# Performance work log

Measured on AMD Instinct MI355X. Metric: run time of the kernel, lower is better.

The kernel has to match this reference:

```python
import jax, jax.numpy as jnp
import numpy as np

HIDDEN = 1024
HEADS = 16
HEAD_DIM = HIDDEN // HEADS


def setup_inputs() -> dict:
    key = jax.random.key(0)
    ks = jax.random.split(key, 9)
    s = 1.0 / np.sqrt(HIDDEN)
    x = jax.random.normal(ks[0], (1, 4096, HIDDEN), dtype=jnp.float32)
    return {
        "x": x,
        "wq": jax.random.normal(ks[1], (HIDDEN, HIDDEN), dtype=jnp.float32) * s,
        "bq": jnp.zeros((HIDDEN,), dtype=jnp.float32),
        "wk": jax.random.normal(ks[2], (HIDDEN, HIDDEN), dtype=jnp.float32) * s,
        "bk": jnp.zeros((HIDDEN,), dtype=jnp.float32),
        "wv": jax.random.normal(ks[3], (HIDDEN, HIDDEN), dtype=jnp.float32) * s,
        "bv": jnp.zeros((HIDDEN,), dtype=jnp.float32),
        "wo": jax.random.normal(ks[4], (HIDDEN, HIDDEN), dtype=jnp.float32) * s,
        "bo": jnp.zeros((HIDDEN,), dtype=jnp.float32),
    }


def reference(x, wq, bq, wk, bk, wv, bv, wo, bo):
    B, S, D = x.shape
    H, Hd = HEADS, HEAD_DIM
    # projections (torch Linear: y = x @ W.T + b)
    q = (x @ wq.T + bq).reshape(B, S, H, Hd).transpose(0, 2, 1, 3)  # [B,H,S,Hd]
    k = (x @ wk.T + bk).reshape(B, S, H, Hd).transpose(0, 2, 1, 3)
    v = (x @ wv.T + bv).reshape(B, S, H, Hd).transpose(0, 2, 1, 3)
    scores = jnp.einsum("bhqd,bhkd->bhqk", q, k) / jnp.sqrt(jnp.float32(Hd))
    attn = jax.nn.softmax(scores, axis=-1)  # full [B,H,S,S] matrix, faithful to source
    out = jnp.einsum("bhqk,bhkd->bhqd", attn, v)  # [B,H,S,Hd]
    out = out.transpose(0, 2, 1, 3).reshape(B, S, D)
    return out @ wo.T + bo
```

## Files before the change

kernel.cpp:

```cpp
#include <hip/hip_runtime.h>
#include <stdint.h>

#define S 4096
#define D 1024
#define H 16
#define HD 64

#define QK_SCALE 0.18033688011112042f

typedef short short8  __attribute__((ext_vector_type(8)));
typedef float floatx4 __attribute__((ext_vector_type(4)));
typedef float floatx16 __attribute__((ext_vector_type(16)));

__device__ __forceinline__ unsigned short f2bf(float f) {
  union { float f; unsigned int i; } x; x.f = f;
  unsigned int r = x.i + 0x7FFFu + ((x.i >> 16) & 1u);
  return (unsigned short)(r >> 16);
}

#if defined(__has_builtin)
#if __has_builtin(__builtin_amdgcn_cvt_pk_bf16_f32)
#define HAVE_PK_BF16 1
#endif
#if __has_builtin(__builtin_amdgcn_exp2f)
#define HAVE_RAW_EXP2 1
#endif
#endif

__device__ __forceinline__ unsigned int pkbf(float a, float b) {
#ifdef HAVE_PK_BF16
  typedef __bf16 bf2_t __attribute__((ext_vector_type(2)));
  bf2_t t = __builtin_amdgcn_cvt_pk_bf16_f32(a, b);
  return __builtin_bit_cast(unsigned int, t);
#else
  return (unsigned int)f2bf(a) | ((unsigned int)f2bf(b) << 16);
#endif
}

__device__ __forceinline__ float fexp2(float x) {
#ifdef HAVE_RAW_EXP2
  return __builtin_amdgcn_exp2f(x);
#else
  return exp2f(x);
#endif
}

__global__ __launch_bounds__(256) void cvt_kernel(
    const float* __restrict__ x,  unsigned short* __restrict__ xb,
    const float* __restrict__ wq, unsigned short* __restrict__ wqb,
    const float* __restrict__ wk, unsigned short* __restrict__ wkb,
    const float* __restrict__ wv, unsigned short* __restrict__ wvb,
    const float* __restrict__ wo, unsigned short* __restrict__ wob,
    const float* __restrict__ bq, float* __restrict__ bqs)
{
  const int z = blockIdx.y;
  const float* s; unsigned short* d;
  float scale = 1.f;
  if (z < 4)       { s = x + (size_t)z * 1048576; d = xb + (size_t)z * 1048576; }
  else if (z == 4) { s = wq; d = wqb; scale = QK_SCALE; }
  else if (z == 5) { s = wk; d = wkb; }
  else if (z == 6) { s = wv; d = wvb; }
  else             { s = wo; d = wob; }
  const size_t i = ((size_t)blockIdx.x * 256 + threadIdx.x) * 4;
  float4 v = *reinterpret_cast<const float4*>(s + i);
  uint2 o;
  o.x = pkbf(v.x * scale, v.y * scale);
  o.y = pkbf(v.z * scale, v.w * scale);
  *reinterpret_cast<uint2*>(d + i) = o;
  if (z == 4 && blockIdx.x == 0) {
    const int t = threadIdx.x;
    #pragma unroll
    for (int j = 0; j < 4; ++j) bqs[t * 4 + j] = bq[t * 4 + j] * QK_SCALE;
  }
}

__global__ __launch_bounds__(256) void gemm_bt(
    const unsigned short* __restrict__ X,
    const unsigned short* __restrict__ W0, const float* __restrict__ B0, unsigned short* __restrict__ C0,
    const unsigned short* __restrict__ W1, const float* __restrict__ B1, unsigned short* __restrict__ C1,
    const unsigned short* __restrict__ W2, const float* __restrict__ B2, unsigned short* __restrict__ C2,
    float* __restrict__ Cf, unsigned short* __restrict__ VtOut)
{
  const unsigned short* W; const float* Bb; unsigned short* C;
  const int z = blockIdx.z;
  if (z == 0)      { W = W0; Bb = B0; C = C0; }
  else if (z == 1) { W = W1; Bb = B1; C = C1; }
  else             { W = W2; Bb = B2; C = C2; }

  const int bm = blockIdx.y, bn = blockIdx.x;
  const int tid  = threadIdx.x;
  const int lane = tid & 63, wave = tid >> 6;
  const int quad = lane >> 4, n16 = lane & 15;
  const int wm = (wave >> 1) * 64, wn = (wave & 1) * 64;

  __shared__ unsigned short As[128 * 40];
  __shared__ unsigned short Bs[128 * 40];
  __shared__ unsigned short Ts[64 * 136];

  floatx4 zero = {0.f, 0.f, 0.f, 0.f};
  floatx4 acc[4][4];
  #pragma unroll
  for (int i = 0; i < 4; ++i)
    #pragma unroll
    for (int j = 0; j < 4; ++j) acc[i][j] = zero;

  const int r1 = tid >> 2, kc = (tid & 3) * 8;
  const unsigned short* Xa = X + (size_t)(bm * 128 + r1) * D + kc;
  const unsigned short* Wa = W + (size_t)(bn * 128 + r1) * D + kc;

  for (int k0 = 0; k0 < D; k0 += 32) {
    __syncthreads();
    uint4 a0 = *reinterpret_cast<const uint4*>(Xa + k0);
    uint4 a1 = *reinterpret_cast<const uint4*>(Xa + (size_t)64 * D + k0);
    uint4 b0 = *reinterpret_cast<const uint4*>(Wa + k0);
    uint4 b1 = *reinterpret_cast<const uint4*>(Wa + (size_t)64 * D + k0);
    *reinterpret_cast<uint4*>(&As[r1 * 40 + kc])        = a0;
    *reinterpret_cast<uint4*>(&As[(r1 + 64) * 40 + kc]) = a1;
    *reinterpret_cast<uint4*>(&Bs[r1 * 40 + kc])        = b0;
    *reinterpret_cast<uint4*>(&Bs[(r1 + 64) * 40 + kc]) = b1;
    __syncthreads();

    short8 af[4], bfr[4];
    #pragma unroll
    for (int t = 0; t < 4; ++t) {
      af[t]  = *reinterpret_cast<const short8*>(&As[(wm + t * 16 + n16) * 40 + quad * 8]);
      bfr[t] = *reinterpret_cast<const short8*>(&Bs[(wn + t * 16 + n16) * 40 + quad * 8]);
    }
    #pragma unroll
    for (int tm = 0; tm < 4; ++tm)
      #pragma unroll
      for (int tn = 0; tn < 4; ++tn)
        acc[tm][tn] = __builtin_amdgcn_mfma_f32_16x16x32_bf16(af[tm], bfr[tn], acc[tm][tn], 0, 0, 0);
  }

  if (z == 2 && VtOut) {
    #pragma unroll
    for (int p = 0; p < 2; ++p) {
      __syncthreads();
      if ((wn >> 6) == p) {
        #pragma unroll
        for (int tn = 0; tn < 4; ++tn) {
          const int col = bn * 128 + p * 64 + tn * 16 + n16;
          const float bias = Bb[col];
          #pragma unroll
          for (int tm = 0; tm < 4; ++tm) {
            uint2 w;
            w.x = pkbf(acc[tm][tn][0] + bias, acc[tm][tn][1] + bias);
            w.y = pkbf(acc[tm][tn][2] + bias, acc[tm][tn][3] + bias);
            *reinterpret_cast<uint2*>(&Ts[(tn * 16 + n16) * 136 + wm + tm * 16 + quad * 4]) = w;
          }
        }
      }
      __syncthreads();
      {
        const int rl = tid >> 2, cc = (tid & 3) * 32;
        uint4 t0 = *reinterpret_cast<const uint4*>(&Ts[rl * 136 + cc]);
        uint4 t1 = *reinterpret_cast<const uint4*>(&Ts[rl * 136 + cc + 8]);
        uint4 t2 = *reinterpret_cast<const uint4*>(&Ts[rl * 136 + cc + 16]);
        uint4 t3 = *reinterpret_cast<const uint4*>(&Ts[rl * 136 + cc + 24]);
        const size_t go = (size_t)(bn * 128 + p * 64 + rl) * S + bm * 128 + cc;
        *reinterpret_cast<uint4*>(&VtOut[go])      = t0;
        *reinterpret_cast<uint4*>(&VtOut[go + 8])  = t1;
        *reinterpret_cast<uint4*>(&VtOut[go + 16]) = t2;
        *reinterpret_cast<uint4*>(&VtOut[go + 24]) = t3;
      }
    }
    return;
  }

  #pragma unroll
  for (int tn = 0; tn < 4; ++tn) {
    const int col = bn * 128 + wn + tn * 16 + n16;
    const float bias = Bb[col];
    #pragma unroll
    for (int tm = 0; tm < 4; ++tm) {
      const int rowb = bm * 128 + wm + tm * 16 + quad * 4;
      #pragma unroll
      for (int r = 0; r < 4; ++r) {
        const float v = acc[tm][tn][r] + bias;
        if (Cf) Cf[(size_t)(rowb + r) * D + col] = v;
        else    C[(size_t)(rowb + r) * D + col]  = f2bf(v);
      }
    }
  }
}

__global__ __launch_bounds__(256, 2) void attn(
    const unsigned short* __restrict__ Q,
    const unsigned short* __restrict__ K,
    const unsigned short* __restrict__ Vt,
    unsigned short* __restrict__ Op,
    float* __restrict__ Ls)
{
  const int h    = blockIdx.y;
  const int z    = blockIdx.z;
  const int q0   = blockIdx.x * 256;
  const int key0 = z * (S / 2);
  const int tid  = threadIdx.x;
  const int lane = tid & 63, wave = tid >> 6;
  const int l31 = lane & 31, h8 = lane >> 5;

  __shared__ unsigned short Ks[64 * 72];
  __shared__ unsigned short Vs[64 * 72];
  __shared__ unsigned short Pq[4][64 * 72];

  const int qA = q0 + wave * 64 + l31;
  const int qB = qA + 32;
  short8 qfA[4], qfB[4];
  #pragma unroll
  for (int ks = 0; ks < 4; ++ks) {
    qfA[ks] = *reinterpret_cast<const short8*>(Q + (size_t)qA * D + h * HD + ks * 16 + h8 * 8);
    qfB[ks] = *reinterpret_cast<const short8*>(Q + (size_t)qB * D + h * HD + ks * 16 + h8 * 8);
  }

  floatx16 oA0 = {}, oA1 = {}, oB0 = {}, oB1 = {};
  float lsumA = 0.f, lsumB = 0.f;

  const int r1 = tid >> 2, c16 = (tid & 3) * 16;
  const unsigned short* Kbase = K  + (size_t)(key0 + r1) * D + h * HD + c16;
  const unsigned short* Vbase = Vt + (size_t)(h * HD + r1) * S + key0 + c16;

  uint4 ka, kb, va, vb;
  ka = *reinterpret_cast<const uint4*>(Kbase);
  kb = *reinterpret_cast<const uint4*>(Kbase + 8);
  va = *reinterpret_cast<const uint4*>(Vbase);
  vb = *reinterpret_cast<const uint4*>(Vbase + 8);

  const int NIT = (S / 2) / 64;
  for (int kt = 0; kt < NIT; ++kt) {
    __syncthreads();
    *reinterpret_cast<uint4*>(&Ks[r1 * 72 + c16])     = ka;
    *reinterpret_cast<uint4*>(&Ks[r1 * 72 + c16 + 8]) = kb;
    *reinterpret_cast<uint4*>(&Vs[r1 * 72 + c16])     = va;
    *reinterpret_cast<uint4*>(&Vs[r1 * 72 + c16 + 8]) = vb;
    __syncthreads();

    const int kn = (kt < NIT - 1) ? kt + 1 : kt;
    ka = *reinterpret_cast<const uint4*>(Kbase + (size_t)kn * 64 * D);
    kb = *reinterpret_cast<const uint4*>(Kbase + (size_t)kn * 64 * D + 8);
    va = *reinterpret_cast<const uint4*>(Vbase + kn * 64);
    vb = *reinterpret_cast<const uint4*>(Vbase + kn * 64 + 8);

    floatx16 sA0 = {}, sA1 = {}, sB0 = {}, sB1 = {};
    #pragma unroll
    for (int ks = 0; ks < 4; ++ks) {
      short8 a0 = *reinterpret_cast<const short8*>(&Ks[l31 * 72 + ks * 16 + h8 * 8]);
      short8 a1 = *reinterpret_cast<const short8*>(&Ks[(32 + l31) * 72 + ks * 16 + h8 * 8]);
      sA0 = __builtin_amdgcn_mfma_f32_32x32x16_bf16(a0, qfA[ks], sA0, 0, 0, 0);
      sA1 = __builtin_amdgcn_mfma_f32_32x32x16_bf16(a1, qfA[ks], sA1, 0, 0, 0);
      sB0 = __builtin_amdgcn_mfma_f32_32x32x16_bf16(a0, qfB[ks], sB0, 0, 0, 0);
      sB1 = __builtin_amdgcn_mfma_f32_32x32x16_bf16(a1, qfB[ks], sB1, 0, 0, 0);
    }

    float rsA = 0.f, rsB = 0.f;
    #pragma unroll
    for (int r = 0; r < 16; ++r) {
      sA0[r] = fexp2(sA0[r]); rsA += sA0[r];
      sA1[r] = fexp2(sA1[r]); rsA += sA1[r];
      sB0[r] = fexp2(sB0[r]); rsB += sB0[r];
      sB1[r] = fexp2(sB1[r]); rsB += sB1[r];
    }
    rsA += __shfl_xor(rsA, 32);
    rsB += __shfl_xor(rsB, 32);
    lsumA += rsA;
    lsumB += rsB;

    unsigned short* pwA = &Pq[wave][l31 * 72];
    unsigned short* pwB = &Pq[wave][(32 + l31) * 72];
    #pragma unroll
    for (int rg = 0; rg < 4; ++rg) {
      uint2 w0, w1;
      w0.x = pkbf(sA0[rg * 4 + 0], sA0[rg * 4 + 1]);
      w0.y = pkbf(sA0[rg * 4 + 2], sA0[rg * 4 + 3]);
      w1.x = pkbf(sA1[rg * 4 + 0], sA1[rg * 4 + 1]);
      w1.y = pkbf(sA1[rg * 4 + 2], sA1[rg * 4 + 3]);
      *reinterpret_cast<uint2*>(&pwA[rg * 8 + h8 * 4])      = w0;
      *reinterpret_cast<uint2*>(&pwA[32 + rg * 8 + h8 * 4]) = w1;
      uint2 v0, v1;
      v0.x = pkbf(sB0[rg * 4 + 0], sB0[rg * 4 + 1]);
      v0.y = pkbf(sB0[rg * 4 + 2], sB0[rg * 4 + 3]);
      v1.x = pkbf(sB1[rg * 4 + 0], sB1[rg * 4 + 1]);
      v1.y = pkbf(sB1[rg * 4 + 2], sB1[rg * 4 + 3]);
      *reinterpret_cast<uint2*>(&pwB[rg * 8 + h8 * 4])      = v0;
      *reinterpret_cast<uint2*>(&pwB[32 + rg * 8 + h8 * 4]) = v1;
    }

    short8 pbA[4], pbB[4];
    #pragma unroll
    for (int ks = 0; ks < 4; ++ks) {
      pbA[ks] = *reinterpret_cast<const short8*>(&Pq[wave][l31 * 72 + ks * 16 + h8 * 8]);
      pbB[ks] = *reinterpret_cast<const short8*>(&Pq[wave][(32 + l31) * 72 + ks * 16 + h8 * 8]);
    }
    #pragma unroll
    for (int ks = 0; ks < 4; ++ks) {
      short8 va0 = *reinterpret_cast<const short8*>(&Vs[l31 * 72 + ks * 16 + h8 * 8]);
      short8 va1 = *reinterpret_cast<const short8*>(&Vs[(32 + l31) * 72 + ks * 16 + h8 * 8]);
      oA0 = __builtin_amdgcn_mfma_f32_32x32x16_bf16(va0, pbA[ks], oA0, 0, 0, 0);
      oA1 = __builtin_amdgcn_mfma_f32_32x32x16_bf16(va1, pbA[ks], oA1, 0, 0, 0);
      oB0 = __builtin_amdgcn_mfma_f32_32x32x16_bf16(va0, pbB[ks], oB0, 0, 0, 0);
      oB1 = __builtin_amdgcn_mfma_f32_32x32x16_bf16(va1, pbB[ks], oB1, 0, 0, 0);
    }
  }

  if (h8 == 0) {
    Ls[(size_t)z * S * H + qA * H + h] = lsumA;
    Ls[(size_t)z * S * H + qB * H + h] = lsumB;
  }

  unsigned short* obA = Op + (size_t)z * S * D + (size_t)qA * D + h * HD;
  unsigned short* obB = Op + (size_t)z * S * D + (size_t)qB * D + h * HD;
  #pragma unroll
  for (int rg = 0; rg < 4; ++rg) {
    uint2 w0, w1;
    w0.x = pkbf(oA0[rg * 4 + 0], oA0[rg * 4 + 1]);
    w0.y = pkbf(oA0[rg * 4 + 2], oA0[rg * 4 + 3]);
    w1.x = pkbf(oA1[rg * 4 + 0], oA1[rg * 4 + 1]);
    w1.y = pkbf(oA1[rg * 4 + 2], oA1[rg * 4 + 3]);
    *reinterpret_cast<uint2*>(&obA[rg * 8 + h8 * 4])      = w0;
    *reinterpret_cast<uint2*>(&obA[32 + rg * 8 + h8 * 4]) = w1;
    uint2 v0, v1;
    v0.x = pkbf(oB0[rg * 4 + 0], oB0[rg * 4 + 1]);
    v0.y = pkbf(oB0[rg * 4 + 2], oB0[rg * 4 + 3]);
    v1.x = pkbf(oB1[rg * 4 + 0], oB1[rg * 4 + 1]);
    v1.y = pkbf(oB1[rg * 4 + 2], oB1[rg * 4 + 3]);
    *reinterpret_cast<uint2*>(&obB[rg * 8 + h8 * 4])      = v0;
    *reinterpret_cast<uint2*>(&obB[32 + rg * 8 + h8 * 4]) = v1;
  }
}

__global__ __launch_bounds__(256) void combine(
    unsigned short* __restrict__ Op,
    const float* __restrict__ Ls)
{
  const size_t e8 = ((size_t)blockIdx.x * 256 + threadIdx.x) * 8;
  const int q = (int)(e8 >> 10);
  const int col = (int)(e8 & 1023);
  const int hh = col >> 6;
  const float l = Ls[q * H + hh] + Ls[S * H + q * H + hh];
  const float inv = 1.f / l;
  uint4 a = *reinterpret_cast<const uint4*>(Op + e8);
  uint4 b = *reinterpret_cast<const uint4*>(Op + (size_t)S * D + e8);
  uint4 r;
  const unsigned int* au = &a.x; const unsigned int* bu = &b.x; unsigned int* ru = &r.x;
  #pragma unroll
  for (int w = 0; w < 4; ++w) {
    union { unsigned int i; float f; } alo, ahi, blo, bhi;
    alo.i = au[w] << 16;          ahi.i = au[w] & 0xFFFF0000u;
    blo.i = bu[w] << 16;          bhi.i = bu[w] & 0xFFFF0000u;
    ru[w] = pkbf((alo.f + blo.f) * inv, (ahi.f + bhi.f) * inv);
  }
  *reinterpret_cast<uint4*>(Op + e8) = r;
}

extern "C" void kernel_launch(void* const* d_in, const int* in_sizes, int n_in,
                              void* d_out, int out_size, void* d_ws, size_t ws_size,
                              hipStream_t stream) {
  const float* x  = (const float*)d_in[0];
  const float* wq = (const float*)d_in[1];
  const float* bq = (const float*)d_in[2];
  const float* wk = (const float*)d_in[3];
  const float* bk = (const float*)d_in[4];
  const float* wv = (const float*)d_in[5];
  const float* bv = (const float*)d_in[6];
  const float* wo = (const float*)d_in[7];
  const float* bo = (const float*)d_in[8];
  float* out = (float*)d_out;

  unsigned short* ws = (unsigned short*)d_ws;
  const size_t SD = (size_t)S * D;
  const size_t DD = (size_t)D * D;
  unsigned short* xb  = ws;
  unsigned short* wqb = xb + SD;
  unsigned short* wkb = wqb + DD;
  unsigned short* wvb = wkb + DD;
  unsigned short* wob = wvb + DD;
  unsigned short* Qw  = wob + DD;
  unsigned short* Kw  = Qw + SD;
  unsigned short* Vtw = Kw + SD;
  unsigned short* Op  = Vtw + SD;
  float* Ls  = (float*)(Op + 2 * SD);
  float* bqs = Ls + 2 * (size_t)S * H;

  dim3 blk(256);
  cvt_kernel<<<dim3(1024, 8), blk, 0, stream>>>(x, xb, wq, wqb, wk, wkb, wv, wvb, wo, wob, bq, bqs);
  gemm_bt<<<dim3(D / 128, S / 128, 3), blk, 0, stream>>>(
      xb, wqb, bqs, Qw, wkb, bk, Kw, wvb, bv, nullptr, nullptr, Vtw);
  attn<<<dim3(S / 256, H, 2), blk, 0, stream>>>(Qw, Kw, Vtw, Op, Ls);
  combine<<<dim3(SD / (256 * 8)), blk, 0, stream>>>(Op, Ls);
  gemm_bt<<<dim3(D / 128, S / 128, 1), blk, 0, stream>>>(
      Op, wob, bo, nullptr, wob, bo, nullptr, wob, bo, nullptr, out, nullptr);
}
```

Measured before the change: 265.3 us.

## Use async global-to-LDS loads in projection GEMM and keep P in registers

The projection GEMM now stages X and W tiles with global_load_lds direct-to-LDS copies instead of loading into registers and then storing to shared memory, and it drops the LDS row padding. The attention kernel removes the per-wave P shared-memory round trip. It packs the softmax probabilities straight from the S accumulators into B-operand registers and permutes the V tile columns in LDS so the key ordering matches. This removes LDS writes, reads and VGPR staging. The unpadded GEMM tiles risk bank conflicts, and there is no explicit vmcnt wait before the barrier, which may be a correctness risk.

Measured after the change: 263.5 us. Within noise of the previous version (-0.7%).

```diff
diff --git a/kernel.cpp b/kernel.cpp
--- a/kernel.cpp
+++ b/kernel.cpp
@@ -43,6 +43,12 @@
 #else
   return exp2f(x);
 #endif
+}
+
+__device__ __forceinline__ void async16(const unsigned short* g, unsigned short* l) {
+  __builtin_amdgcn_global_load_lds(
+      (const __attribute__((address_space(1))) unsigned int*)g,
+      (__attribute__((address_space(3))) unsigned int*)l, 16, 0, 0);
 }
 
 __global__ __launch_bounds__(256) void cvt_kernel(
@@ -93,8 +99,8 @@
   const int quad = lane >> 4, n16 = lane & 15;
   const int wm = (wave >> 1) * 64, wn = (wave & 1) * 64;
 
-  __shared__ unsigned short As[128 * 40];
-  __shared__ unsigned short Bs[128 * 40];
+  __shared__ unsigned short As[128 * 32];
+  __shared__ unsigned short Bs[128 * 32];
   __shared__ unsigned short Ts[64 * 136];
 
   floatx4 zero = {0.f, 0.f, 0.f, 0.f};
@@ -104,27 +110,28 @@
     #pragma unroll
     for (int j = 0; j < 4; ++j) acc[i][j] = zero;
 
-  const int r1 = tid >> 2, kc = (tid & 3) * 8;
-  const unsigned short* Xa = X + (size_t)(bm * 128 + r1) * D + kc;
-  const unsigned short* Wa = W + (size_t)(bn * 128 + r1) * D + kc;
+  const int srow = 16 * wave + (lane >> 2);
+  const int scol = (lane & 3) * 8;
+  const unsigned short* XaL = X + (size_t)(bm * 128 + srow) * D + scol;
+  const unsigned short* WaL = W + (size_t)(bn * 128 + srow) * D + scol;
+  unsigned short* ldsA0 = &As[(16 * wave) * 32];
+  unsigned short* ldsA1 = &As[(64 + 16 * wave) * 32];
+  unsigned short* ldsB0 = &Bs[(16 * wave) * 32];
+  unsigned short* ldsB1 = &Bs[(64 + 16 * wave) * 32];
 
   for (int k0 = 0; k0 < D; k0 += 32) {
     __syncthreads();
-    uint4 a0 = *reinterpret_cast<const uint4*>(Xa + k0);
-    uint4 a1 = *reinterpret_cast<const uint4*>(Xa + (size_t)64 * D + k0);
-    uint4 b0 = *reinterpret_cast<const uint4*>(Wa + k0);
-    uint4 b1 = *reinterpret_cast<const uint4*>(Wa + (size_t)64 * D + k0);
-    *reinterpret_cast<uint4*>(&As[r1 * 40 + kc])        = a0;
-    *reinterpret_cast<uint4*>(&As[(r1 + 64) * 40 + kc]) = a1;
-    *reinterpret_cast<uint4*>(&Bs[r1 * 40 + kc])        = b0;
-    *reinterpret_cast<uint4*>(&Bs[(r1 + 64) * 40 + kc]) = b1;
+    async16(XaL + k0, ldsA0);
+    async16(XaL + (size_t)64 * D + k0, ldsA1);
+    async16(WaL + k0, ldsB0);
+    async16(WaL + (size_t)64 * D + k0, ldsB1);
     __syncthreads();
 
     short8 af[4], bfr[4];
     #pragma unroll
     for (int t = 0; t < 4; ++t) {
-      af[t]  = *reinterpret_cast<const short8*>(&As[(wm + t * 16 + n16) * 40 + quad * 8]);
-      bfr[t] = *reinterpret_cast<const short8*>(&Bs[(wn + t * 16 + n16) * 40 + quad * 8]);
+      af[t]  = *reinterpret_cast<const short8*>(&As[(wm + t * 16 + n16) * 32 + quad * 8]);
+      bfr[t] = *reinterpret_cast<const short8*>(&Bs[(wn + t * 16 + n16) * 32 + quad * 8]);
     }
     #pragma unroll
     for (int tm = 0; tm < 4; ++tm)
@@ -202,7 +209,6 @@
 
   __shared__ unsigned short Ks[64 * 72];
   __shared__ unsigned short Vs[64 * 72];
-  __shared__ unsigned short Pq[4][64 * 72];
 
   const int qA = q0 + wave * 64 + l31;
   const int qB = qA + 32;
@@ -231,8 +237,17 @@
     __syncthreads();
     *reinterpret_cast<uint4*>(&Ks[r1 * 72 + c16])     = ka;
     *reinterpret_cast<uint4*>(&Ks[r1 * 72 + c16 + 8]) = kb;
-    *reinterpret_cast<uint4*>(&Vs[r1 * 72 + c16])     = va;
-    *reinterpret_cast<uint4*>(&Vs[r1 * 72 + c16 + 8]) = vb;
+    {
+      uint2 w;
+      w.x = va.x; w.y = va.y;
+      *reinterpret_cast<uint2*>(&Vs[r1 * 72 + c16 + 0])  = w;
+      w.x = va.z; w.y = va.w;
+      *reinterpret_cast<uint2*>(&Vs[r1 * 72 + c16 + 8])  = w;
+      w.x = vb.x; w.y = vb.y;
+      *reinterpret_cast<uint2*>(&Vs[r1 * 72 + c16 + 4])  = w;
+      w.x = vb.z; w.y = vb.w;
+      *reinterpret_cast<uint2*>(&Vs[r1 * 72 + c16 + 12]) = w;
+    }
     __syncthreads();
 
     const int kn = (kt < NIT - 1) ? kt + 1 : kt;
@@ -265,32 +280,19 @@
     lsumA += rsA;
     lsumB += rsB;
 
-    unsigned short* pwA = &Pq[wave][l31 * 72];
-    unsigned short* pwB = &Pq[wave][(32 + l31) * 72];
-    #pragma unroll
-    for (int rg = 0; rg < 4; ++rg) {
-      uint2 w0, w1;
-      w0.x = pkbf(sA0[rg * 4 + 0], sA0[rg * 4 + 1]);
-      w0.y = pkbf(sA0[rg * 4 + 2], sA0[rg * 4 + 3]);
-      w1.x = pkbf(sA1[rg * 4 + 0], sA1[rg * 4 + 1]);
-      w1.y = pkbf(sA1[rg * 4 + 2], sA1[rg * 4 + 3]);
-      *reinterpret_cast<uint2*>(&pwA[rg * 8 + h8 * 4])      = w0;
-      *reinterpret_cast<uint2*>(&pwA[32 + rg * 8 + h8 * 4]) = w1;
-      uint2 v0, v1;
-      v0.x = pkbf(sB0[rg * 4 + 0], sB0[rg * 4 + 1]);
-      v0.y = pkbf(sB0[rg * 4 + 2], sB0[rg * 4 + 3]);
-      v1.x = pkbf(sB1[rg * 4 + 0], sB1[rg * 4 + 1]);
-      v1.y = pkbf(sB1[rg * 4 + 2], sB1[rg * 4 + 3]);
-      *reinterpret_cast<uint2*>(&pwB[rg * 8 + h8 * 4])      = v0;
-      *reinterpret_cast<uint2*>(&pwB[32 + rg * 8 + h8 * 4]) = v1;
-    }
-
     short8 pbA[4], pbB[4];
-    #pragma unroll
-    for (int ks = 0; ks < 4; ++ks) {
-      pbA[ks] = *reinterpret_cast<const short8*>(&Pq[wave][l31 * 72 + ks * 16 + h8 * 8]);
-      pbB[ks] = *reinterpret_cast<const short8*>(&Pq[wave][(32 + l31) * 72 + ks * 16 + h8 * 8]);
-    }
+    {
+      unsigned int* ua = reinterpret_cast<unsigned int*>(pbA);
+      unsigned int* ub = reinterpret_cast<unsigned int*>(pbB);
+      #pragma unroll
+      for (int i = 0; i < 8; ++i) {
+        ua[i]     = pkbf(sA0[2 * i], sA0[2 * i + 1]);
+        ua[8 + i] = pkbf(sA1[2 * i], sA1[2 * i + 1]);
+        ub[i]     = pkbf(sB0[2 * i], sB0[2 * i + 1]);
+        ub[8 + i] = pkbf(sB1[2 * i], sB1[2 * i + 1]);
+      }
+    }
+
     #pragma unroll
     for (int ks = 0; ks < 4; ++ks) {
       short8 va0 = *reinterpret_cast<const short8*>(&Vs[l31 * 72 + ks * 16 + h8 * 8]);
```
